# Optimization experiments

Measured on AMD Instinct MI355X. Metric: run time of the kernel, lower is better.

Reference implementation:

```python
import jax, jax.numpy as jnp
import numpy as np

NUM_NODES = 10000
NUM_EDGES = 640000
D_IN = 128
D_OUT = 128


def setup_inputs() -> dict:
    key = jax.random.key(0)
    k1, k2, k3 = jax.random.split(key, 3)
    x = jax.random.normal(k1, (NUM_NODES, D_IN), dtype=jnp.float32)
    edge_index = jax.random.randint(k2, (2, NUM_EDGES), 0, NUM_NODES, dtype=jnp.int32)
    W = jax.random.normal(k3, (D_IN, D_OUT), dtype=jnp.float32) / np.sqrt(D_IN)
    bias = jnp.zeros((D_OUT,), dtype=jnp.float32)
    return {"x": x, "edge_index": edge_index, "W": W, "bias": bias}


def reference(x, edge_index, W, bias):
    num_nodes = x.shape[0]
    # add self-loops
    self_loops = jnp.arange(num_nodes, dtype=edge_index.dtype)
    row = jnp.concatenate([edge_index[0], self_loops])
    col = jnp.concatenate([edge_index[1], self_loops])
    # symmetric normalization D^{-1/2} A D^{-1/2} (degree computed over row)
    deg = jax.ops.segment_sum(jnp.ones_like(row, dtype=jnp.float32), row,
                              num_segments=num_nodes)
    deg_inv_sqrt = jnp.power(deg, -0.5)
    deg_inv_sqrt = jnp.where(jnp.isinf(deg_inv_sqrt), 0.0, deg_inv_sqrt)
    edge_weight = deg_inv_sqrt[row] * deg_inv_sqrt[col]  # [E+N]
    # linear projection (no bias)
    h = x @ W  # [N, D_OUT]
    # gather -> scale -> scatter-sum
    messages = h[row] * edge_weight[:, None]  # [E+N, D_OUT]
    out = jax.ops.segment_sum(messages, col, num_segments=num_nodes)
    return out + bias
```

## Files before the change

### kernel.cpp

```cpp
#include <hip/hip_runtime.h>


#define NNODES 10000
#define NB 64
#define HBLOCK 1024
#define STAGE_CAP 256

__device__ inline unsigned short f2bf(float f) {
    union { float f; unsigned u; } v; v.f = f;
    unsigned r = v.u + 0x7FFFu + ((v.u >> 16) & 1u);
    return (unsigned short)(r >> 16);
}
__device__ inline float bf2f_lo(unsigned u) {
    union { unsigned u; float f; } v; v.u = u << 16; return v.f;
}
__device__ inline float bf2f_hi(unsigned u) {
    union { unsigned u; float f; } v; v.u = u & 0xFFFF0000u; return v.f;
}

__global__ __launch_bounds__(HBLOCK) void histsort_gemm_kernel(
    const int* __restrict__ row, const int* __restrict__ col,
    const float* __restrict__ x, const float* __restrict__ W,
    unsigned* __restrict__ meta, int* __restrict__ outdeg,
    unsigned short* __restrict__ blkcsr, unsigned short* __restrict__ g,
    int N, int E, int EPB) {
    __shared__ int hmem[NNODES];
    __shared__ unsigned short loff16[NNODES];
    __shared__ int wsum[16];
    const int tid = threadIdx.x;

    if (blockIdx.x < NB) {
        const int b = blockIdx.x;
        for (int j = tid; j < NNODES; j += HBLOCK) hmem[j] = 0;
        __syncthreads();
        const int e0 = b * EPB, e1 = min(E, e0 + EPB);
        const int span = e1 - e0;
        const bool vec4 = ((((size_t)(row + e0)) | ((size_t)(col + e0))) & 15) == 0;
        const int nq = vec4 ? (span >> 2) : 0;
        const int4* __restrict__ r4p = (const int4*)(row + e0);
        const int4* __restrict__ c4p = (const int4*)(col + e0);
        for (int qi = tid; qi < nq; qi += HBLOCK) {
            int4 r4 = r4p[qi], c4 = c4p[qi];
            atomicAdd((unsigned*)&hmem[r4.x], 1u);
            atomicAdd((unsigned*)&hmem[r4.y], 1u);
            atomicAdd((unsigned*)&hmem[r4.z], 1u);
            atomicAdd((unsigned*)&hmem[r4.w], 1u);
            atomicAdd((unsigned*)&hmem[c4.x], 0x10000u);
            atomicAdd((unsigned*)&hmem[c4.y], 0x10000u);
            atomicAdd((unsigned*)&hmem[c4.z], 0x10000u);
            atomicAdd((unsigned*)&hmem[c4.w], 0x10000u);
        }
        for (int e = e0 + nq * 4 + tid; e < e1; e += HBLOCK) {
            atomicAdd((unsigned*)&hmem[row[e]], 1u);
            atomicAdd((unsigned*)&hmem[col[e]], 0x10000u);
        }
        __syncthreads();
        {
            const int lane = tid & 63, wid = tid >> 6;
            const int i0 = tid * 10;
            const int i1 = min(NNODES, i0 + 10);
            int s = 0;
            for (int i = i0; i < i1; ++i) s += (int)(((unsigned)hmem[i]) >> 16);
            int p = s;
#pragma unroll
            for (int d = 1; d < 64; d <<= 1) {
                int y = __shfl_up(p, d);
                if (lane >= d) p += y;
            }
            if (lane == 63) wsum[wid] = p;
            __syncthreads();
            if (tid < 16) {
                int v = wsum[tid];
#pragma unroll
                for (int d = 1; d < 16; d <<= 1) {
                    int y = __shfl_up(v, d);
                    if (tid >= d) v += y;
                }
                wsum[tid] = v;
            }
            __syncthreads();
            int run = (wid ? wsum[wid - 1] : 0) + (p - s);
            for (int i = i0; i < i1; ++i) {
                loff16[i] = (unsigned short)run;
                run += (int)(((unsigned)hmem[i]) >> 16);
            }
        }
        __syncthreads();
        for (int j = tid; j < NNODES; j += HBLOCK) {
            unsigned v = (unsigned)hmem[j];
            unsigned cnt = v >> 16;
            unsigned lo = (unsigned)loff16[j];
            meta[(size_t)j * NB + b] = lo | (cnt << 16);
            int od = (int)(v & 0xFFFFu);
            if (od) atomicAdd(&outdeg[j], od);
            hmem[j] = (int)lo;
        }
        __syncthreads();
        unsigned short* __restrict__ bc = blkcsr + (size_t)b * EPB;
        for (int qi = tid; qi < nq; qi += HBLOCK) {
            int4 r4 = r4p[qi], c4 = c4p[qi];
            int s0 = atomicAdd(&hmem[c4.x], 1);
            bc[s0] = (unsigned short)r4.x;
            int s1 = atomicAdd(&hmem[c4.y], 1);
            bc[s1] = (unsigned short)r4.y;
            int s2 = atomicAdd(&hmem[c4.z], 1);
            bc[s2] = (unsigned short)r4.z;
            int s3 = atomicAdd(&hmem[c4.w], 1);
            bc[s3] = (unsigned short)r4.w;
        }
        for (int e = e0 + nq * 4 + tid; e < e1; e += HBLOCK) {
            int slot = atomicAdd(&hmem[col[e]], 1);
            bc[slot] = (unsigned short)row[e];
        }
    } else {
        float* xs = (float*)hmem;
        const int rowBase = (blockIdx.x - NB) * 32;
        {
            int r = rowBase + (tid >> 5);
            float4 v = make_float4(0.f, 0.f, 0.f, 0.f);
            if (r < N) v = ((const float4*)x)[rowBase * 32 + tid];
            ((float4*)xs)[tid] = v;
        }
        __syncthreads();
        const int lr = tid >> 5, c4 = tid & 31;
        const int rr = rowBase + lr;
        const float4* __restrict__ W4 = (const float4*)W;
        float4 acc = make_float4(0.f, 0.f, 0.f, 0.f);
#pragma unroll 8
        for (int k = 0; k < 128; ++k) {
            float xv = xs[lr * 128 + k];
            float4 wv = W4[k * 32 + c4];
            acc.x = fmaf(xv, wv.x, acc.x);
            acc.y = fmaf(xv, wv.y, acc.y);
            acc.z = fmaf(xv, wv.z, acc.z);
            acc.w = fmaf(xv, wv.w, acc.w);
        }
        if (rr < N) {
            ushort4 o;
            o.x = f2bf(acc.x);
            o.y = f2bf(acc.y);
            o.z = f2bf(acc.z);
            o.w = f2bf(acc.w);
            ((ushort4*)g)[rr * 32 + c4] = o;
        }
    }
}

__global__ __launch_bounds__(256) void gather_kernel(
    const int* __restrict__ outdeg, const unsigned* __restrict__ meta,
    const unsigned short* __restrict__ blkcsr,
    const unsigned short* __restrict__ g, const float* __restrict__ bias,
    float* __restrict__ out, int N, int EPB) {
    __shared__ unsigned short stage[4][STAGE_CAP];
    __shared__ float dstage[4][STAGE_CAP];
    const int wv = threadIdx.x >> 6;
    const int lane = threadIdx.x & 63;
    const int c = (int)((blockIdx.x * blockDim.x + threadIdx.x) >> 6);
    const bool act = (c < N);

    unsigned m = act ? meta[(size_t)c * NB + lane] : 0u;
    int sl = (int)(m & 0xFFFFu);
    int cn = (int)(m >> 16);
    int p = cn;
#pragma unroll
    for (int d = 1; d < 64; d <<= 1) {
        int y = __shfl_up(p, d);
        if (lane >= d) p += y;
    }
    int excl = p - cn;
    int L = __shfl(p, 63);
    if (act && cn) {
        const unsigned short* seg = blkcsr + (size_t)lane * EPB + sl;
        for (int k = 0; k < cn; ++k) {
            int r = (int)seg[k];
            stage[wv][excl + k] = (unsigned short)r;
            dstage[wv][excl + k] = rsqrtf(1.0f + (float)outdeg[r]);
        }
    }
    __syncthreads();
    if (!act) return;

    const int q = lane >> 4;
    const int l16 = lane & 15;
    const uint4* __restrict__ g4 = (const uint4*)g;
    const float dc = rsqrtf(1.0f + (float)outdeg[c]);

    float al0 = 0.f, ah0 = 0.f, al1 = 0.f, ah1 = 0.f;
    float al2 = 0.f, ah2 = 0.f, al3 = 0.f, ah3 = 0.f;

    if (q == 0) {
        uint4 w = g4[(size_t)c * 16 + l16];
        al0 = fmaf(bf2f_lo(w.x), dc, al0); ah0 = fmaf(bf2f_hi(w.x), dc, ah0);
        al1 = fmaf(bf2f_lo(w.y), dc, al1); ah1 = fmaf(bf2f_hi(w.y), dc, ah1);
        al2 = fmaf(bf2f_lo(w.z), dc, al2); ah2 = fmaf(bf2f_hi(w.z), dc, ah2);
        al3 = fmaf(bf2f_lo(w.w), dc, al3); ah3 = fmaf(bf2f_hi(w.w), dc, ah3);
    }

    for (int base = 0; base < L; base += 64) {
        int cnt = min(64, L - base);
#pragma unroll
        for (int t = 0; t < 64; t += 4) {
            int j = t + q;
            if (j < cnt) {
                int r = (int)stage[wv][base + j];
                float ds = dstage[wv][base + j];
                uint4 w = g4[(size_t)r * 16 + l16];
                al0 = fmaf(bf2f_lo(w.x), ds, al0); ah0 = fmaf(bf2f_hi(w.x), ds, ah0);
                al1 = fmaf(bf2f_lo(w.y), ds, al1); ah1 = fmaf(bf2f_hi(w.y), ds, ah1);
                al2 = fmaf(bf2f_lo(w.z), ds, al2); ah2 = fmaf(bf2f_hi(w.z), ds, ah2);
                al3 = fmaf(bf2f_lo(w.w), ds, al3); ah3 = fmaf(bf2f_hi(w.w), ds, ah3);
            }
        }
    }
    al0 += __shfl(al0, lane ^ 32); ah0 += __shfl(ah0, lane ^ 32);
    al1 += __shfl(al1, lane ^ 32); ah1 += __shfl(ah1, lane ^ 32);
    al2 += __shfl(al2, lane ^ 32); ah2 += __shfl(ah2, lane ^ 32);
    al3 += __shfl(al3, lane ^ 32); ah3 += __shfl(ah3, lane ^ 32);
    al0 += __shfl(al0, lane ^ 16); ah0 += __shfl(ah0, lane ^ 16);
    al1 += __shfl(al1, lane ^ 16); ah1 += __shfl(ah1, lane ^ 16);
    al2 += __shfl(al2, lane ^ 16); ah2 += __shfl(ah2, lane ^ 16);
    al3 += __shfl(al3, lane ^ 16); ah3 += __shfl(ah3, lane ^ 16);

    if (lane < 32) {
        int oi = ((lane & 15) << 1) | (lane >> 4);
        float4 bv = ((const float4*)bias)[oi];
        float4 o;
        if (lane < 16) {
            o.x = fmaf(al0, dc, bv.x);
            o.y = fmaf(ah0, dc, bv.y);
            o.z = fmaf(al1, dc, bv.z);
            o.w = fmaf(ah1, dc, bv.w);
        } else {
            o.x = fmaf(al2, dc, bv.x);
            o.y = fmaf(ah2, dc, bv.y);
            o.z = fmaf(al3, dc, bv.z);
            o.w = fmaf(ah3, dc, bv.w);
        }
        ((float4*)out)[(size_t)c * 32 + oi] = o;
    }
}

extern "C" void kernel_launch(void* const* d_in, const int* in_sizes, int n_in,
                              void* d_out, int out_size, void* d_ws, size_t ws_size,
                              hipStream_t stream) {
    const float* x    = (const float*)d_in[0];
    const int*   ei   = (const int*)d_in[1];
    const float* W    = (const float*)d_in[2];
    const float* bias = (const float*)d_in[3];
    float* out = (float*)d_out;

    int N = in_sizes[0] / 128;
    int E = in_sizes[1] / 2;
    const int* row = ei;
    const int* col = ei + E;
    int EPB = (E + NB - 1) / NB;

    auto align256 = [](size_t v) { return (v + 255) & ~(size_t)255; };
    char* p = (char*)d_ws;
    int*            outdeg = (int*)p;            p += align256((size_t)N * 4);
    unsigned*       meta   = (unsigned*)p;       p += align256((size_t)N * NB * 4);
    unsigned short* blkcsr = (unsigned short*)p; p += align256((size_t)NB * EPB * 2);
    unsigned short* g      = (unsigned short*)p; p += align256((size_t)N * 128 * 2);

    hipMemsetAsync(outdeg, 0, (size_t)N * 4, stream);

    int gemmBlocks = (N + 31) / 32;
    histsort_gemm_kernel<<<NB + gemmBlocks, HBLOCK, 0, stream>>>(
        row, col, x, W, meta, outdeg, blkcsr, g, N, E, EPB);

    int gBlocks = (N + 3) / 4;
    gather_kernel<<<gBlocks, 256, 0, stream>>>(
        outdeg, meta, blkcsr, g, bias, out, N, EPB);
}
```

Baseline: 122.6 us.

## Register-tile GEMM blocks over 128 rows and transpose meta layout

The GEMM part now processes 128 rows per block with x transposed into padded shared memory, and each thread computes a 4x4 register tile instead of 1x4. This raises arithmetic reuse of W loads and cuts the number of GEMM blocks. The meta array is also transposed to block-major so the histogram blocks write contiguous rows, though the gather kernel's per-lane reads become strided across NNODES. Shared memory is unioned into one buffer sized for the larger x tile.

Result: faster. 109.1 us (-11.0%).

```diff
diff --git a/kernel.cpp b/kernel.cpp
--- a/kernel.cpp
+++ b/kernel.cpp
@@ -5,6 +5,8 @@
 #define NB 64
 #define HBLOCK 1024
 #define STAGE_CAP 256
+#define GROWS 128
+#define XPAD 132
 
 __device__ inline unsigned short f2bf(float f) {
     union { float f; unsigned u; } v; v.f = f;
@@ -24,9 +26,11 @@
     unsigned* __restrict__ meta, int* __restrict__ outdeg,
     unsigned short* __restrict__ blkcsr, unsigned short* __restrict__ g,
     int N, int E, int EPB) {
-    __shared__ int hmem[NNODES];
-    __shared__ unsigned short loff16[NNODES];
-    __shared__ int wsum[16];
+    __shared__ __align__(16) char smem[GROWS * XPAD * 4];
+    int* hmem = (int*)smem;
+    unsigned short* loff16 = (unsigned short*)(smem + 40000);
+    int* wsum = (int*)(smem + 60000);
+    float* xs = (float*)smem;
     const int tid = threadIdx.x;
 
     if (blockIdx.x < NB) {
@@ -90,7 +94,7 @@
             unsigned v = (unsigned)hmem[j];
             unsigned cnt = v >> 16;
             unsigned lo = (unsigned)loff16[j];
-            meta[(size_t)j * NB + b] = lo | (cnt << 16);
+            meta[(size_t)b * NNODES + j] = lo | (cnt << 16);
             int od = (int)(v & 0xFFFFu);
             if (od) atomicAdd(&outdeg[j], od);
             hmem[j] = (int)lo;
@@ -113,35 +117,68 @@
             bc[slot] = (unsigned short)row[e];
         }
     } else {
-        float* xs = (float*)hmem;
-        const int rowBase = (blockIdx.x - NB) * 32;
+        const int rowBase = (blockIdx.x - NB) * GROWS;
         {
-            int r = rowBase + (tid >> 5);
-            float4 v = make_float4(0.f, 0.f, 0.f, 0.f);
-            if (r < N) v = ((const float4*)x)[rowBase * 32 + tid];
-            ((float4*)xs)[tid] = v;
-        }
-        __syncthreads();
-        const int lr = tid >> 5, c4 = tid & 31;
-        const int rr = rowBase + lr;
+            const float4* __restrict__ x4g = (const float4*)x;
+#pragma unroll
+            for (int i = 0; i < 4; ++i) {
+                int idx = tid + i * HBLOCK;
+                int c16 = idx & 31;
+                int r = idx >> 5;
+                int gr = rowBase + r;
+                float4 v = make_float4(0.f, 0.f, 0.f, 0.f);
+                if (gr < N) v = x4g[(size_t)gr * 32 + c16];
+                xs[(c16 * 4 + 0) * XPAD + r] = v.x;
+                xs[(c16 * 4 + 1) * XPAD + r] = v.y;
+                xs[(c16 * 4 + 2) * XPAD + r] = v.z;
+                xs[(c16 * 4 + 3) * XPAD + r] = v.w;
+            }
+        }
+        __syncthreads();
+        const int w = tid >> 6, lane = tid & 63;
+        const int aa = w >> 1, bb = w & 1;
+        const int rg = aa * 4 + (lane >> 4);
+        const int c4 = bb * 16 + (lane & 15);
         const float4* __restrict__ W4 = (const float4*)W;
-        float4 acc = make_float4(0.f, 0.f, 0.f, 0.f);
-#pragma unroll 8
+        float4 acc0 = make_float4(0.f, 0.f, 0.f, 0.f);
+        float4 acc1 = make_float4(0.f, 0.f, 0.f, 0.f);
+        float4 acc2 = make_float4(0.f, 0.f, 0.f, 0.f);
+        float4 acc3 = make_float4(0.f, 0.f, 0.f, 0.f);
+#pragma unroll 4
         for (int k = 0; k < 128; ++k) {
-            float xv = xs[lr * 128 + k];
+            float4 xv = *(const float4*)&xs[k * XPAD + rg * 4];
             float4 wv = W4[k * 32 + c4];
-            acc.x = fmaf(xv, wv.x, acc.x);
-            acc.y = fmaf(xv, wv.y, acc.y);
-            acc.z = fmaf(xv, wv.z, acc.z);
-            acc.w = fmaf(xv, wv.w, acc.w);
-        }
-        if (rr < N) {
-            ushort4 o;
-            o.x = f2bf(acc.x);
-            o.y = f2bf(acc.y);
-            o.z = f2bf(acc.z);
-            o.w = f2bf(acc.w);
-            ((ushort4*)g)[rr * 32 + c4] = o;
+            acc0.x = fmaf(xv.x, wv.x, acc0.x);
+            acc0.y = fmaf(xv.x, wv.y, acc0.y);
+            acc0.z = fmaf(xv.x, wv.z, acc0.z);
+            acc0.w = fmaf(xv.x, wv.w, acc0.w);
+            acc1.x = fmaf(xv.y, wv.x, acc1.x);
+            acc1.y = fmaf(xv.y, wv.y, acc1.y);
+            acc1.z = fmaf(xv.y, wv.z, acc1.z);
+            acc1.w = fmaf(xv.y, wv.w, acc1.w);
+            acc2.x = fmaf(xv.z, wv.x, acc2.x);
+            acc2.y = fmaf(xv.z, wv.y, acc2.y);
+            acc2.z = fmaf(xv.z, wv.z, acc2.z);
+            acc2.w = fmaf(xv.z, wv.w, acc2.w);
+            acc3.x = fmaf(xv.w, wv.x, acc3.x);
+            acc3.y = fmaf(xv.w, wv.y, acc3.y);
+            acc3.z = fmaf(xv.w, wv.z, acc3.z);
+            acc3.w = fmaf(xv.w, wv.w, acc3.w);
+        }
+        ushort4* __restrict__ g4 = (ushort4*)g;
+        const int r0 = rowBase + rg * 4;
+        float4 accs[4] = { acc0, acc1, acc2, acc3 };
+#pragma unroll
+        for (int i = 0; i < 4; ++i) {
+            int gr = r0 + i;
+            if (gr < N) {
+                ushort4 o;
+                o.x = f2bf(accs[i].x);
+                o.y = f2bf(accs[i].y);
+                o.z = f2bf(accs[i].z);
+                o.w = f2bf(accs[i].w);
+                g4[(size_t)gr * 32 + c4] = o;
+            }
         }
     }
 }
@@ -158,7 +195,7 @@
     const int c = (int)((blockIdx.x * blockDim.x + threadIdx.x) >> 6);
     const bool act = (c < N);
 
-    unsigned m = act ? meta[(size_t)c * NB + lane] : 0u;
+    unsigned m = act ? meta[(size_t)lane * NNODES + c] : 0u;
     int sl = (int)(m & 0xFFFFu);
     int cn = (int)(m >> 16);
     int p = cn;
@@ -258,13 +295,13 @@
     auto align256 = [](size_t v) { return (v + 255) & ~(size_t)255; };
     char* p = (char*)d_ws;
     int*            outdeg = (int*)p;            p += align256((size_t)N * 4);
-    unsigned*       meta   = (unsigned*)p;       p += align256((size_t)N * NB * 4);
+    unsigned*       meta   = (unsigned*)p;       p += align256((size_t)NB * N * 4);
     unsigned short* blkcsr = (unsigned short*)p; p += align256((size_t)NB * EPB * 2);
     unsigned short* g      = (unsigned short*)p; p += align256((size_t)N * 128 * 2);
 
     hipMemsetAsync(outdeg, 0, (size_t)N * 4, stream);
 
-    int gemmBlocks = (N + 31) / 32;
+    int gemmBlocks = (N + GROWS - 1) / GROWS;
     histsort_gemm_kernel<<<NB + gemmBlocks, HBLOCK, 0, stream>>>(
         row, col, x, W, meta, outdeg, blkcsr, g, N, E, EPB);
 
```
